# Kernel tuning notes

Hardware: AMD Instinct MI355X
Metric: run time of the kernel (lower is better)

The kernel has to match this reference:

```python
import jax, jax.numpy as jnp
import numpy as np


def _feature_vol(ref, tgt, maxdisp):
    """Vectorized diff cost volume.
    ref, tgt: [B, C, H, W]. Returns cost: [B, C, D, H, W] with
    cost[:, :, d, :, w] = |ref[:, :, :, w] - tgt[:, :, :, w-d]| for w >= d, else 0.
    Matches the torch loop: cost[:,:,i,:,i:] = |ref[:,:,:,i:] - tgt[:,:,:,:W-i]|.
    """
    B, C, H, W = ref.shape
    d = jnp.arange(maxdisp)[:, None]          # [D, 1]
    w = jnp.arange(W)[None, :]                # [1, W]
    idx = jnp.maximum(w - d, 0)               # [D, W] gather index into target width
    valid = (w >= d).astype(ref.dtype)        # [D, W]
    # gather shifted target: [B, C, H, D, W] -> [B, C, D, H, W]
    tgt_s = jnp.transpose(tgt[:, :, :, idx], (0, 1, 3, 2, 4))
    cost = jnp.abs(ref[:, :, None, :, :] - tgt_s) * valid[None, None, :, None, :]
    return cost


def setup_inputs() -> dict:
    key = jax.random.key(0)
    k1, k2 = jax.random.split(key)
    B, C, H, W = 4, 32, 80, 160
    refimg_fea = jax.random.normal(k1, (B, C, H, W), dtype=jnp.float32)
    targetimg_fea = jax.random.normal(k2, (B, C, H, W), dtype=jnp.float32)
    return {"refimg_fea": refimg_fea, "targetimg_fea": targetimg_fea, "maxdisp": 24}


def reference(refimg_fea, targetimg_fea, maxdisp):
    # diff cost volume [B, C, D, H, W]
    cost = _feature_vol(refimg_fea, targetimg_fea, maxdisp)
    # aggregate channels -> [B, D, H, W] (stand-in for the 3D decoder head's 1-ch output)
    cost_agg = cost.sum(axis=1)
    prob = jax.nn.softmax(cost_agg, axis=1)
    disp = jnp.arange(maxdisp, dtype=prob.dtype)
    pred = jnp.einsum('bdhw,d->bhw', prob, disp)  # [B, H, W]
    return pred
```

## Files before the change

### kernel.cpp

```cpp
#include <hip/hip_runtime.h>
#include <math.h>

#define BB 4
#define CC 32
#define HH 80
#define WW 160
#define DD 24

#define WT 32
#define NT (WW / WT)
#define HALO 24
#define SWW (WT + HALO)
#define NDG 6
#define NCQ 4
#define CPQ (CC / NCQ)
#define NTH (8 * NDG * NCQ)

__device__ __forceinline__ void gload_lds16(const void* g, void* l) {
    __builtin_amdgcn_global_load_lds(
        (const __attribute__((address_space(1))) void*)g,
        (__attribute__((address_space(3))) void*)l,
        16, 0, 0);
}

__global__ __launch_bounds__(NTH) void hsm_fused_kernel(
    const float* __restrict__ ref,
    const float* __restrict__ tgt,
    float* __restrict__ out) {

    __shared__ __align__(16) float s_tgt[CC * SWW];
    __shared__ __align__(16) float s_ref[CC * WT];
    __shared__ __align__(16) float s_p[3 * DD * WT];

    const int blk  = blockIdx.x;
    const int tile = blk % NT;
    const int row  = blk / NT;
    const int b    = row / HH;
    const int h    = row % HH;
    const int w0   = tile * WT;
    const int tid  = threadIdx.x;
    const int wave = tid >> 6;
    const int lane = tid & 63;

    const float* tgt_row = tgt + ((size_t)b * CC * HH + h) * WW;
    const float* ref_row = ref + ((size_t)b * CC * HH + h) * WW;

    for (int q = wave; q < 11; q += 3) {
        if (q < 7) {
            const int f4 = (q << 6) + lane;
            const int c  = f4 / 14;
            const int j4 = f4 - 14 * c;
            int gw = w0 - HALO + 4 * j4;
            if (gw < 0) gw = 0;
            gload_lds16(tgt_row + (size_t)c * (HH * WW) + gw, &s_tgt[q << 8]);
        } else {
            const int f4 = ((q - 7) << 6) + lane;
            const int c  = f4 >> 3;
            const int j4 = f4 & 7;
            gload_lds16(ref_row + (size_t)c * (HH * WW) + w0 + (j4 << 2),
                        &s_ref[(q - 7) << 8]);
        }
    }

    const int w4 = tid & 7;
    const int t3 = tid >> 3;
    const int dg = t3 % NDG;
    const int cq = t3 / NDG;

    float acc[4][4];
#pragma unroll
    for (int k = 0; k < 4; ++k)
#pragma unroll
        for (int j = 0; j < 4; ++j) acc[k][j] = 0.0f;

    const int tbase = 4 * (w4 - dg) + (HALO - 4);
    const int rbase = 4 * w4;

    __syncthreads();

    if (w0 != 0) {
#pragma unroll 4
        for (int cc = 0; cc < CPQ; ++cc) {
            const int c = cq * CPQ + cc;
            const float4 r  = *(const float4*)&s_ref[c * WT + rbase];
            const float4 t0 = *(const float4*)&s_tgt[c * SWW + tbase];
            const float4 t1 = *(const float4*)&s_tgt[c * SWW + tbase + 4];
            const float rr[4] = {r.x, r.y, r.z, r.w};
            const float w8[8] = {t0.x, t0.y, t0.z, t0.w, t1.x, t1.y, t1.z, t1.w};
#pragma unroll
            for (int k = 0; k < 4; ++k)
#pragma unroll
                for (int j = 0; j < 4; ++j)
                    acc[k][j] += fabsf(rr[j] - w8[j - k + 4]);
        }
    } else {
#pragma unroll 4
        for (int cc = 0; cc < CPQ; ++cc) {
            const int c = cq * CPQ + cc;
            const float4 r  = *(const float4*)&s_ref[c * WT + rbase];
            const float4 t0 = *(const float4*)&s_tgt[c * SWW + tbase];
            const float4 t1 = *(const float4*)&s_tgt[c * SWW + tbase + 4];
            const float rr[4] = {r.x, r.y, r.z, r.w};
            const float w8[8] = {t0.x, t0.y, t0.z, t0.w, t1.x, t1.y, t1.z, t1.w};
#pragma unroll
            for (int k = 0; k < 4; ++k)
#pragma unroll
                for (int j = 0; j < 4; ++j)
                    if (4 * w4 + j >= 4 * dg + k)
                        acc[k][j] += fabsf(rr[j] - w8[j - k + 4]);
        }
    }

    float4* p4 = (float4*)s_p;
    if (cq != 0) {
#pragma unroll
        for (int k = 0; k < 4; ++k) {
            const int d = 4 * dg + k;
            p4[((cq - 1) * DD + d) * 8 + w4] =
                make_float4(acc[k][0], acc[k][1], acc[k][2], acc[k][3]);
        }
    }
    __syncthreads();
    if (cq == 0) {
#pragma unroll
        for (int k = 0; k < 4; ++k) {
            const int d = 4 * dg + k;
            const float4 a   = p4[(0 * DD + d) * 8 + w4];
            const float4 bb  = p4[(1 * DD + d) * 8 + w4];
            const float4 cc4 = p4[(2 * DD + d) * 8 + w4];
            p4[(0 * DD + d) * 8 + w4] = make_float4(
                acc[k][0] + a.x + bb.x + cc4.x,
                acc[k][1] + a.y + bb.y + cc4.y,
                acc[k][2] + a.z + bb.z + cc4.z,
                acc[k][3] + a.w + bb.w + cc4.w);
        }
    }
    __syncthreads();

    if (tid < WT) {
        float a[DD];
#pragma unroll
        for (int d = 0; d < DD; ++d) a[d] = s_p[d * WT + tid];
        float t[12];
#pragma unroll
        for (int d = 0; d < 12; ++d) t[d] = fmaxf(a[d], a[d + 12]);
#pragma unroll
        for (int d = 0; d < 6; ++d) t[d] = fmaxf(t[d], t[d + 6]);
        const float m = fmaxf(fmaxf(fmaxf(t[0], t[1]), fmaxf(t[2], t[3])),
                              fmaxf(t[4], t[5]));
        float den0 = 0.0f, num0 = 0.0f, den1 = 0.0f, num1 = 0.0f;
#pragma unroll
        for (int d = 0; d < DD; d += 2) {
            const float e0 = __expf(a[d] - m);
            const float e1 = __expf(a[d + 1] - m);
            den0 += e0;  num0 += (float)d * e0;
            den1 += e1;  num1 += (float)(d + 1) * e1;
        }
        out[(size_t)row * WW + w0 + tid] = (num0 + num1) / (den0 + den1);
    }
}

extern "C" void kernel_launch(void* const* d_in, const int* in_sizes, int n_in,
                              void* d_out, int out_size, void* d_ws, size_t ws_size,
                              hipStream_t stream) {
    const float* ref = (const float*)d_in[0];
    const float* tgt = (const float*)d_in[1];
    float* out = (float*)d_out;

    hsm_fused_kernel<<<BB * HH * NT, NTH, 0, stream>>>(ref, tgt, out);
}
```

Baseline: 69.49 us.

## Split channel loads into two stages and reduce partials with warp shuffles

Result: no change. 70.80 us (+1.9%).

```diff
diff --git a/kernel.cpp b/kernel.cpp
--- a/kernel.cpp
+++ b/kernel.cpp
@@ -11,10 +11,7 @@
 #define NT (WW / WT)
 #define HALO 24
 #define SWW (WT + HALO)
-#define NDG 6
-#define NCQ 4
-#define CPQ (CC / NCQ)
-#define NTH (8 * NDG * NCQ)
+#define NTH 192
 
 __device__ __forceinline__ void gload_lds16(const void* g, void* l) {
     __builtin_amdgcn_global_load_lds(
@@ -30,7 +27,7 @@
 
     __shared__ __align__(16) float s_tgt[CC * SWW];
     __shared__ __align__(16) float s_ref[CC * WT];
-    __shared__ __align__(16) float s_p[3 * DD * WT];
+    __shared__ __align__(16) float s_p[DD * WT];
 
     const int blk  = blockIdx.x;
     const int tile = blk % NT;
@@ -45,7 +42,7 @@
     const float* tgt_row = tgt + ((size_t)b * CC * HH + h) * WW;
     const float* ref_row = ref + ((size_t)b * CC * HH + h) * WW;
 
-    for (int q = wave; q < 11; q += 3) {
+    auto issue = [&](int q) {
         if (q < 7) {
             const int f4 = (q << 6) + lane;
             const int c  = f4 / 14;
@@ -60,12 +57,17 @@
             gload_lds16(ref_row + (size_t)c * (HH * WW) + w0 + (j4 << 2),
                         &s_ref[(q - 7) << 8]);
         }
-    }
+    };
+    if (wave == 0)      { issue(0); issue(3); issue(4); issue(9);  }
+    else if (wave == 1) { issue(1); issue(7); issue(5); issue(10); }
+    else                { issue(2); issue(8); issue(6); }
 
     const int w4 = tid & 7;
-    const int t3 = tid >> 3;
-    const int dg = t3 % NDG;
-    const int cq = t3 / NDG;
+    const int cq = (tid >> 3) & 3;
+    const int dg = tid >> 5;
+
+    const int tbase = 4 * (w4 - dg) + (HALO - 4);
+    const int rbase = 4 * w4;
 
     float acc[4][4];
 #pragma unroll
@@ -73,15 +75,10 @@
 #pragma unroll
         for (int j = 0; j < 4; ++j) acc[k][j] = 0.0f;
 
-    const int tbase = 4 * (w4 - dg) + (HALO - 4);
-    const int rbase = 4 * w4;
-
-    __syncthreads();
-
-    if (w0 != 0) {
-#pragma unroll 4
-        for (int cc = 0; cc < CPQ; ++cc) {
-            const int c = cq * CPQ + cc;
+    auto computeN = [&](int cc0) {
+#pragma unroll
+        for (int i = 0; i < 4; ++i) {
+            const int c = cq + 4 * (cc0 + i);
             const float4 r  = *(const float4*)&s_ref[c * WT + rbase];
             const float4 t0 = *(const float4*)&s_tgt[c * SWW + tbase];
             const float4 t1 = *(const float4*)&s_tgt[c * SWW + tbase + 4];
@@ -93,10 +90,11 @@
                 for (int j = 0; j < 4; ++j)
                     acc[k][j] += fabsf(rr[j] - w8[j - k + 4]);
         }
-    } else {
-#pragma unroll 4
-        for (int cc = 0; cc < CPQ; ++cc) {
-            const int c = cq * CPQ + cc;
+    };
+    auto computeB = [&](int cc0) {
+#pragma unroll
+        for (int i = 0; i < 4; ++i) {
+            const int c = cq + 4 * (cc0 + i);
             const float4 r  = *(const float4*)&s_ref[c * WT + rbase];
             const float4 t0 = *(const float4*)&s_tgt[c * SWW + tbase];
             const float4 t1 = *(const float4*)&s_tgt[c * SWW + tbase + 4];
@@ -109,31 +107,37 @@
                     if (4 * w4 + j >= 4 * dg + k)
                         acc[k][j] += fabsf(rr[j] - w8[j - k + 4]);
         }
-    }
+    };
 
-    float4* p4 = (float4*)s_p;
-    if (cq != 0) {
+    if (wave < 2) asm volatile("s_waitcnt vmcnt(2)" ::: "memory");
+    else          asm volatile("s_waitcnt vmcnt(1)" ::: "memory");
+    __builtin_amdgcn_s_barrier();
+    __builtin_amdgcn_sched_barrier(0);
+
+    if (w0 != 0) computeN(0); else computeB(0);
+
+    asm volatile("s_waitcnt vmcnt(0)" ::: "memory");
+    __builtin_amdgcn_s_barrier();
+    __builtin_amdgcn_sched_barrier(0);
+
+    if (w0 != 0) computeN(4); else computeB(4);
+
 #pragma unroll
-        for (int k = 0; k < 4; ++k) {
-            const int d = 4 * dg + k;
-            p4[((cq - 1) * DD + d) * 8 + w4] =
+    for (int k = 0; k < 4; ++k)
+#pragma unroll
+        for (int j = 0; j < 4; ++j) {
+            float v = acc[k][j];
+            v += __shfl_xor(v, 8);
+            v += __shfl_xor(v, 16);
+            acc[k][j] = v;
+        }
+
+    if (cq == 0) {
+        float4* p4 = (float4*)s_p;
+#pragma unroll
+        for (int k = 0; k < 4; ++k)
+            p4[(4 * dg + k) * 8 + w4] =
                 make_float4(acc[k][0], acc[k][1], acc[k][2], acc[k][3]);
-        }
-    }
-    __syncthreads();
-    if (cq == 0) {
-#pragma unroll
-        for (int k = 0; k < 4; ++k) {
-            const int d = 4 * dg + k;
-            const float4 a   = p4[(0 * DD + d) * 8 + w4];
-            const float4 bb  = p4[(1 * DD + d) * 8 + w4];
-            const float4 cc4 = p4[(2 * DD + d) * 8 + w4];
-            p4[(0 * DD + d) * 8 + w4] = make_float4(
-                acc[k][0] + a.x + bb.x + cc4.x,
-                acc[k][1] + a.y + bb.y + cc4.y,
-                acc[k][2] + a.z + bb.z + cc4.z,
-                acc[k][3] + a.w + bb.w + cc4.w);
-        }
     }
     __syncthreads();
 
```
